# Optimization experiments

Hardware: AMD Instinct MI355X
Metric: run time of the kernel (lower is better)

The kernel has to match this reference:

```python
import jax, jax.numpy as jnp
import numpy as np

IMAGE_W = 256
IMAGE_H = 256
EPS = 1e-07
SIGMA2 = 2.0 * 0.1 ** 2  # 2 * sigma^2 with sigma = 0.1


def _norm(x, eps=EPS):
    # min/max over stroke dim (axis=1), per batch
    mn = x.min(axis=1, keepdims=True)
    mx = x.max(axis=1, keepdims=True)
    return (x - mn) / (mx - mn + eps)


def setup_inputs() -> dict:
    key = jax.random.key(0)
    k1, k2 = jax.random.split(key)
    brushes = jax.random.uniform(k1, (16, 64, 2), dtype=jnp.float32)
    patches = jax.random.normal(k2, (16, 64, 3, 32, 32), dtype=jnp.float32)
    return {"brushes": brushes, "patches": patches}


def reference(brushes, patches):
    B, N, _ = brushes.shape
    C, ph, pw = patches.shape[2], patches.shape[3], patches.shape[4]
    w, h = IMAGE_W, IMAGE_H
    pad = ph // 2  # 'half_patch'

    gx = _norm(brushes[:, :, 0]) * w  # [B, N]
    gy = _norm(brushes[:, :, 1]) * h

    # grid coordinates (original builds 2D index arrays whose columns are identical;
    # a 1D arange is the equivalent efficient form)
    a = jnp.arange(w + 2 * pad, dtype=jnp.float32) - pad  # [w+2p]
    b = jnp.arange(h + 2 * pad, dtype=jnp.float32) - pad  # [h+2p]
    widths = jnp.arange(1, pw + 1, dtype=jnp.float32)
    heights = jnp.arange(1, ph + 1, dtype=jnp.float32)

    ux = gx[:, :, None] + (widths - pw / 2 - 0.5)   # [B, N, pw]
    uy = gy[:, :, None] + (heights - pw / 2 - 0.4)  # [B, N, ph] (pw/2 offset as in source)

    # separable Gaussian filter banks, normalized over the padded spatial axis
    Fx = jnp.exp(-((a[None, None, :, None] - ux[:, :, None, :]) ** 2) / SIGMA2)  # [B,N,w+2p,pw]
    Fx = Fx / (Fx.sum(axis=2, keepdims=True) + EPS)
    Fx = Fx[:, :, pad:-pad]  # [B, N, w, pw]

    Fy = jnp.exp(-((b[None, None, :, None] - uy[:, :, None, :]) ** 2) / SIGMA2)  # [B,N,h+2p,ph]
    Fy = Fy / (Fy.sum(axis=2, keepdims=True) + EPS)
    Fy = Fy[:, :, pad:-pad]  # [B, N, h, ph]

    # separable splat: out[b,c,y,x] = mean_n sum_{p,q} Fy[b,n,y,p] Fx[b,n,x,q] patches[b,n,c,p,q]
    t = jnp.einsum('bnxq,bncpq->bncxp', Fx, patches)  # [B,N,C,w,ph]
    out = jnp.einsum('bncxp,bnyp->bcyx', t, Fy) / N   # mean over strokes -> [B,C,h,w]
    return out
```

## Files before the change

### kernel.cpp

```cpp
#include <hip/hip_runtime.h>

#define IMG_W 256
#define IMG_H 256
#define EPSN 1e-7f
#define NS 50.0f
#define NB 16
#define NN 64
#define NC 3
#define PH 32
#define PW 32
#define WIN 36
#define PR 12
#define RST 56

#define TILE_W 64
#define TILE_H 8
#define TPI 128
#define NWG (NB * TPI)

__global__ __launch_bounds__(192)
void fused_kernel(const float* __restrict__ brushes,
                  const float* __restrict__ patches,
                  float* __restrict__ out) {
    __shared__ float2 gxy_s[NN];
    __shared__ int    sPack[NN];
    __shared__ int    sCnt;
    __shared__ float  patch_s[NC * PR * RST];

    int blk = blockIdx.x;
    blk = (blk & 7) * (NWG >> 3) + (blk >> 3);

    const int b    = blk >> 7;
    const int t7   = blk & 127;
    const int ty0  = (t7 >> 2) * TILE_H;
    const int tx0  = (t7 & 3) * TILE_W;
    const int tid  = threadIdx.x;
    const int cc   = tid >> 6;
    const int lane = tid & 63;
    const int ysub = lane >> 4;
    const int xgrp = lane & 15;
    const int ax0  = tx0 + xgrp * 4;
    const int ay0  = ty0 + ysub * 2;

    if (tid < 64) {
        float2 v = ((const float2*)brushes)[b * NN + tid];
        float mnx = v.x, mxx = v.x, mny = v.y, mxy = v.y;
        #pragma unroll
        for (int off = 32; off > 0; off >>= 1) {
            mnx = fminf(mnx, __shfl_xor(mnx, off));
            mxx = fmaxf(mxx, __shfl_xor(mxx, off));
            mny = fminf(mny, __shfl_xor(mny, off));
            mxy = fmaxf(mxy, __shfl_xor(mxy, off));
        }
        float gx = (v.x - mnx) / (mxx - mnx + EPSN) * (float)IMG_W;
        float gy = (v.y - mny) / (mxy - mny + EPSN) * (float)IMG_H;
        gxy_s[tid] = make_float2(gx, gy);

        int ix0 = (int)floorf(gx) - 17;
        int iy0 = (int)floorf(gy) - 17;
        bool ov = (ix0 <= tx0 + TILE_W - 1) && (ix0 + WIN - 1 >= tx0) &&
                  (iy0 <= ty0 + TILE_H - 1) && (iy0 + WIN - 1 >= ty0);
        unsigned long long mask = __ballot(ov);
        if (ov) {
            int pos = __popcll(mask & ((1ull << tid) - 1));
            sPack[pos] = tid;
        }
        if (tid == 0) sCnt = (int)__popcll(mask);
    }
    for (int u = tid; u < NC * PR * 24; u += 192) {
        int row = u / 24, rem = u - row * 24;
        int j = (rem < 8) ? rem : rem + 32;
        patch_s[row * RST + j] = 0.f;
    }
    __syncthreads();
    const int cnt = sCnt;

    float acc[2][4];
    #pragma unroll
    for (int j = 0; j < 2; ++j)
        #pragma unroll
        for (int o = 0; o < 4; ++o) acc[j][o] = 0.f;

    for (int i = 0; i < cnt; ++i) {
        const int n = sPack[i];
        const float2 g = gxy_s[n];

        const float zy0 = (float)ty0 - g.y + 15.4f;
        const int pbase = (int)floorf(zy0) - 1;

        for (int u = tid; u < NC * PR * 8; u += 192) {
            int c  = u / (PR * 8);
            int rm = u - c * (PR * 8);
            int r  = rm >> 3, q4 = (rm & 7) << 2;
            int src = pbase + r;
            float4 v = make_float4(0.f, 0.f, 0.f, 0.f);
            if (src >= 0 && src <= 31)
                v = *(const float4*)(patches +
                      ((size_t)(b * NN + n) * NC + c) * (PH * PW) + src * PW + q4);
            *(float4*)&patch_s[(c * PR + r) * RST + 8 + q4] = v;
        }
        __syncthreads();

        const float zx0 = (float)ax0 - g.x + 15.5f;
        const int   q00 = (int)floorf(zx0) - 1;

        if (q00 >= -6 && q00 <= 31) {
            const float phx = zx0 - floorf(zx0);
            float Ex[4], W[4];
            #pragma unroll
            for (int k = 0; k < 4; ++k) {
                float d = phx + (float)(1 - k);
                Ex[k] = __expf(-NS * d * d);
            }
            float Sx  = ((Ex[0] + Ex[1]) + (Ex[2] + Ex[3]));
            float Dxc = 1.f / (Sx + EPSN);
            #pragma unroll
            for (int k = 0; k < 4; ++k) W[k] = Ex[k] * Dxc;

            const int qbj = (q00 + 8) & ~3;
            const int m   = (q00 + 8) & 3;

            float t[5][4];
            auto rows = [&](auto Mc) {
                constexpr int M = Mc.value;
                #pragma unroll
                for (int rr = 0; rr < 5; ++rr) {
                    const float* rp = &patch_s[(cc * PR + 2 * ysub + rr) * RST + qbj];
                    float4 A  = *(const float4*)(rp);
                    float4 Bv = *(const float4*)(rp + 4);
                    float4 Cv = *(const float4*)(rp + 8);
                    float pv[12] = {A.x, A.y, A.z, A.w, Bv.x, Bv.y, Bv.z, Bv.w,
                                    Cv.x, Cv.y, Cv.z, Cv.w};
                    #pragma unroll
                    for (int o = 0; o < 4; ++o)
                        t[rr][o] = W[0] * pv[M + o]     + W[1] * pv[M + o + 1]
                                 + W[2] * pv[M + o + 2] + W[3] * pv[M + o + 3];
                }
            };
            switch (m) {
                case 0: rows(std::integral_constant<int, 0>{}); break;
                case 1: rows(std::integral_constant<int, 1>{}); break;
                case 2: rows(std::integral_constant<int, 2>{}); break;
                default: rows(std::integral_constant<int, 3>{}); break;
            }

            if (g.x > 255.0f) {
                float cx31 = g.x + 15.5f;
                float dc   = 272.f - cx31;
                float c272 = __expf(-NS * dc * dc);
                float dD   = 1.f / (Sx - c272 + EPSN) - Dxc;
                float e31[4];
                #pragma unroll
                for (int o = 0; o < 4; ++o) {
                    float d = zx0 + (float)o - 31.f;
                    e31[o] = __expf(-NS * d * d) * dD;
                }
                #pragma unroll
                for (int rr = 0; rr < 5; ++rr) {
                    float p31 = patch_s[(cc * PR + 2 * ysub + rr) * RST + 8 + 31];
                    #pragma unroll
                    for (int o = 0; o < 4; ++o) t[rr][o] += e31[o] * p31;
                }
            }

            const float psy = zy0 - floorf(zy0);
            float Ey[4];
            #pragma unroll
            for (int k = 0; k < 4; ++k) {
                float d = psy + (float)(1 - k);
                Ey[k] = __expf(-NS * d * d);
            }
            float Sy  = ((Ey[0] + Ey[1]) + (Ey[2] + Ey[3]));
            float Dyc = (1.f / (Sy + EPSN)) * (1.f / (float)NN);
            float wyA[4], wyB[4];
            #pragma unroll
            for (int k = 0; k < 4; ++k) { wyA[k] = Ey[k] * Dyc; wyB[k] = wyA[k]; }
            if (g.y > 254.9f) {
                float cy31 = g.y + 15.6f;
                float dc   = 272.f - cy31;
                float c272 = __expf(-NS * dc * dc);
                float Dy31 = (1.f / (Sy - c272 + EPSN)) * (1.f / (float)NN);
                #pragma unroll
                for (int k = 0; k < 4; ++k) {
                    if (pbase + 2 * ysub + 0 + k == 31) wyA[k] = Ey[k] * Dy31;
                    if (pbase + 2 * ysub + 1 + k == 31) wyB[k] = Ey[k] * Dy31;
                }
            }

            #pragma unroll
            for (int o = 0; o < 4; ++o) {
                acc[0][o] += wyA[0] * t[0][o] + wyA[1] * t[1][o]
                           + wyA[2] * t[2][o] + wyA[3] * t[3][o];
                acc[1][o] += wyB[0] * t[1][o] + wyB[1] * t[2][o]
                           + wyB[2] * t[3][o] + wyB[3] * t[4][o];
            }
        }
        __syncthreads();
    }

    #pragma unroll
    for (int j = 0; j < 2; ++j) {
        float* o = out + (((size_t)b * NC + cc) * IMG_H + ay0 + j) * IMG_W + ax0;
        *(float4*)o = make_float4(acc[j][0], acc[j][1], acc[j][2], acc[j][3]);
    }
}

extern "C" void kernel_launch(void* const* d_in, const int* in_sizes, int n_in,
                              void* d_out, int out_size, void* d_ws, size_t ws_size,
                              hipStream_t stream) {
    const float* brushes = (const float*)d_in[0];
    const float* patches = (const float*)d_in[1];
    float* out = (float*)d_out;

    fused_kernel<<<NWG, 192, 0, stream>>>(brushes, patches, out);
}
```

Before: 28.56 us.

## Read patch rows directly from global memory instead of staging in LDS

Removes the per-stroke shared-memory staging of patch rows and the two block barriers per stroke. Each thread now loads its float4 patch segments straight from global memory (served by cache) with clamped indices and zero masks to handle out-of-range columns and rows. The compacted stroke list now also stores coordinates to skip one indirection. This trades barrier and LDS traffic for redundant global/L1 loads across threads.

New measurement: 27.91 us. -2.3%, faster.

```diff
diff --git a/kernel.cpp b/kernel.cpp
--- a/kernel.cpp
+++ b/kernel.cpp
@@ -1,4 +1,5 @@
 #include <hip/hip_runtime.h>
+#include <type_traits>
 
 #define IMG_W 256
 #define IMG_H 256
@@ -10,9 +11,6 @@
 #define PH 32
 #define PW 32
 #define WIN 36
-#define PR 12
-#define RST 56
-
 #define TILE_W 64
 #define TILE_H 8
 #define TPI 128
@@ -22,10 +20,9 @@
 void fused_kernel(const float* __restrict__ brushes,
                   const float* __restrict__ patches,
                   float* __restrict__ out) {
-    __shared__ float2 gxy_s[NN];
-    __shared__ int    sPack[NN];
+    __shared__ float2 sG[NN];
+    __shared__ int    sN[NN];
     __shared__ int    sCnt;
-    __shared__ float  patch_s[NC * PR * RST];
 
     int blk = blockIdx.x;
     blk = (blk & 7) * (NWG >> 3) + (blk >> 3);
@@ -54,7 +51,6 @@
         }
         float gx = (v.x - mnx) / (mxx - mnx + EPSN) * (float)IMG_W;
         float gy = (v.y - mny) / (mxy - mny + EPSN) * (float)IMG_H;
-        gxy_s[tid] = make_float2(gx, gy);
 
         int ix0 = (int)floorf(gx) - 17;
         int iy0 = (int)floorf(gy) - 17;
@@ -63,14 +59,10 @@
         unsigned long long mask = __ballot(ov);
         if (ov) {
             int pos = __popcll(mask & ((1ull << tid) - 1));
-            sPack[pos] = tid;
+            sN[pos] = tid;
+            sG[pos] = make_float2(gx, gy);
         }
         if (tid == 0) sCnt = (int)__popcll(mask);
-    }
-    for (int u = tid; u < NC * PR * 24; u += 192) {
-        int row = u / 24, rem = u - row * 24;
-        int j = (rem < 8) ? rem : rem + 32;
-        patch_s[row * RST + j] = 0.f;
     }
     __syncthreads();
     const int cnt = sCnt;
@@ -81,26 +73,15 @@
         #pragma unroll
         for (int o = 0; o < 4; ++o) acc[j][o] = 0.f;
 
+    const float* Pcb = patches + (size_t)b * NN * (NC * PH * PW) + cc * (PH * PW);
+
     for (int i = 0; i < cnt; ++i) {
-        const int n = sPack[i];
-        const float2 g = gxy_s[n];
+        const float2 g = sG[i];
+        const int    n = sN[i];
+        const float* Pc = Pcb + (size_t)n * (NC * PH * PW);
 
         const float zy0 = (float)ty0 - g.y + 15.4f;
         const int pbase = (int)floorf(zy0) - 1;
-
-        for (int u = tid; u < NC * PR * 8; u += 192) {
-            int c  = u / (PR * 8);
-            int rm = u - c * (PR * 8);
-            int r  = rm >> 3, q4 = (rm & 7) << 2;
-            int src = pbase + r;
-            float4 v = make_float4(0.f, 0.f, 0.f, 0.f);
-            if (src >= 0 && src <= 31)
-                v = *(const float4*)(patches +
-                      ((size_t)(b * NN + n) * NC + c) * (PH * PW) + src * PW + q4);
-            *(float4*)&patch_s[(c * PR + r) * RST + 8 + q4] = v;
-        }
-        __syncthreads();
-
         const float zx0 = (float)ax0 - g.x + 15.5f;
         const int   q00 = (int)floorf(zx0) - 1;
 
@@ -117,27 +98,36 @@
             #pragma unroll
             for (int k = 0; k < 4; ++k) W[k] = Ex[k] * Dxc;
 
-            const int qbj = (q00 + 8) & ~3;
-            const int m   = (q00 + 8) & 3;
+            const int qg = ((q00 + 8) & ~3) - 8;
+            const int M  = (q00 + 8) & 3;
+            const int s1 = qg + 4, s2 = qg + 8;
+            const float m0 = (qg >= 0 && qg <= 28) ? 1.f : 0.f;
+            const float m1 = (s1 >= 0 && s1 <= 28) ? 1.f : 0.f;
+            const float m2 = (s2 >= 0 && s2 <= 28) ? 1.f : 0.f;
+            const int c0 = min(max(qg, 0), 28);
+            const int c1 = min(max(s1, 0), 28);
+            const int c2 = min(max(s2, 0), 28);
 
             float t[5][4];
             auto rows = [&](auto Mc) {
-                constexpr int M = Mc.value;
+                constexpr int Mv = Mc.value;
                 #pragma unroll
                 for (int rr = 0; rr < 5; ++rr) {
-                    const float* rp = &patch_s[(cc * PR + 2 * ysub + rr) * RST + qbj];
-                    float4 A  = *(const float4*)(rp);
-                    float4 Bv = *(const float4*)(rp + 4);
-                    float4 Cv = *(const float4*)(rp + 8);
-                    float pv[12] = {A.x, A.y, A.z, A.w, Bv.x, Bv.y, Bv.z, Bv.w,
-                                    Cv.x, Cv.y, Cv.z, Cv.w};
+                    int src = min(max(pbase + 2 * ysub + rr, 0), 31);
+                    const float* rp = Pc + (src << 5);
+                    float4 A  = *(const float4*)(rp + c0);
+                    float4 Bv = *(const float4*)(rp + c1);
+                    float4 Cv = *(const float4*)(rp + c2);
+                    float pv[12] = {A.x * m0, A.y * m0, A.z * m0, A.w * m0,
+                                    Bv.x * m1, Bv.y * m1, Bv.z * m1, Bv.w * m1,
+                                    Cv.x * m2, Cv.y * m2, Cv.z * m2, Cv.w * m2};
                     #pragma unroll
                     for (int o = 0; o < 4; ++o)
-                        t[rr][o] = W[0] * pv[M + o]     + W[1] * pv[M + o + 1]
-                                 + W[2] * pv[M + o + 2] + W[3] * pv[M + o + 3];
+                        t[rr][o] = W[0] * pv[Mv + o]     + W[1] * pv[Mv + o + 1]
+                                 + W[2] * pv[Mv + o + 2] + W[3] * pv[Mv + o + 3];
                 }
             };
-            switch (m) {
+            switch (M) {
                 case 0: rows(std::integral_constant<int, 0>{}); break;
                 case 1: rows(std::integral_constant<int, 1>{}); break;
                 case 2: rows(std::integral_constant<int, 2>{}); break;
@@ -157,7 +147,8 @@
                 }
                 #pragma unroll
                 for (int rr = 0; rr < 5; ++rr) {
-                    float p31 = patch_s[(cc * PR + 2 * ysub + rr) * RST + 8 + 31];
+                    int src = min(max(pbase + 2 * ysub + rr, 0), 31);
+                    float p31 = Pc[(src << 5) + 31];
                     #pragma unroll
                     for (int o = 0; o < 4; ++o) t[rr][o] += e31[o] * p31;
                 }
@@ -170,21 +161,22 @@
                 float d = psy + (float)(1 - k);
                 Ey[k] = __expf(-NS * d * d);
             }
-            float Sy  = ((Ey[0] + Ey[1]) + (Ey[2] + Ey[3]));
-            float Dyc = (1.f / (Sy + EPSN)) * (1.f / (float)NN);
-            float wyA[4], wyB[4];
-            #pragma unroll
-            for (int k = 0; k < 4; ++k) { wyA[k] = Ey[k] * Dyc; wyB[k] = wyA[k]; }
+            float Sy   = ((Ey[0] + Ey[1]) + (Ey[2] + Ey[3]));
+            float DyC  = (1.f / (Sy + EPSN)) * (1.0f / (float)NN);
+            float Dy31 = DyC;
             if (g.y > 254.9f) {
                 float cy31 = g.y + 15.6f;
                 float dc   = 272.f - cy31;
                 float c272 = __expf(-NS * dc * dc);
-                float Dy31 = (1.f / (Sy - c272 + EPSN)) * (1.f / (float)NN);
-                #pragma unroll
-                for (int k = 0; k < 4; ++k) {
-                    if (pbase + 2 * ysub + 0 + k == 31) wyA[k] = Ey[k] * Dy31;
-                    if (pbase + 2 * ysub + 1 + k == 31) wyB[k] = Ey[k] * Dy31;
-                }
+                Dy31 = (1.f / (Sy - c272 + EPSN)) * (1.0f / (float)NN);
+            }
+            float wyA[4], wyB[4];
+            #pragma unroll
+            for (int k = 0; k < 4; ++k) {
+                int rA = pbase + 2 * ysub + k;
+                int rB = rA + 1;
+                wyA[k] = ((unsigned)rA < 32u) ? Ey[k] * ((rA == 31) ? Dy31 : DyC) : 0.f;
+                wyB[k] = ((unsigned)rB < 32u) ? Ey[k] * ((rB == 31) ? Dy31 : DyC) : 0.f;
             }
 
             #pragma unroll
@@ -195,7 +187,6 @@
                            + wyB[2] * t[3][o] + wyB[3] * t[4][o];
             }
         }
-        __syncthreads();
     }
 
     #pragma unroll
```
